# Optimization experiments

Hardware: AMD Instinct MI355X
Metric: run time of the kernel (lower is better)

## Reference

```python
import jax, jax.numpy as jnp
import numpy as np

NUM_HEADS = 16


def setup_inputs() -> dict:
    key = jax.random.key(0)
    k1, k2, k3, k4 = jax.random.split(key, 4)
    B, S, D = 2, 2048, 1024
    x = jax.random.normal(k1, (B, S, D), dtype=jnp.float32)
    W_qkv = jax.random.normal(k2, (D, 3 * D), dtype=jnp.float32) * (1.0 / np.sqrt(D))
    b_qkv = jax.random.normal(k3, (3 * D,), dtype=jnp.float32) * 0.02
    W_out = jax.random.normal(k4, (D, D), dtype=jnp.float32) * (1.0 / np.sqrt(D))
    return {"x": x, "W_qkv": W_qkv, "b_qkv": b_qkv, "W_out": W_out}


def reference(x, W_qkv, b_qkv, W_out):
    B, S, D = x.shape
    H = NUM_HEADS
    Hd = D // H
    scale = 1.0 / np.sqrt(Hd)

    qkv = x @ W_qkv + b_qkv                      # [B, S, 3D]
    q, k, v = jnp.split(qkv, 3, axis=-1)
    # [B, H, S, Hd]
    q = q.reshape(B, S, H, Hd).transpose(0, 2, 1, 3)
    k = k.reshape(B, S, H, Hd).transpose(0, 2, 1, 3)
    v = v.reshape(B, S, H, Hd).transpose(0, 2, 1, 3)

    scores = jnp.einsum('bhqd,bhkd->bhqk', q, k) * scale  # [B, H, S, S]
    causal = jnp.triu(jnp.full((S, S), -jnp.inf, dtype=scores.dtype), k=1)
    scores = scores + causal
    attn = jax.nn.softmax(scores.astype(jnp.float32), axis=-1).astype(q.dtype)

    ctx = jnp.einsum('bhqk,bhkd->bhqd', attn, v)           # [B, H, S, Hd]
    ctx = ctx.transpose(0, 2, 1, 3).reshape(B, S, D)
    return ctx @ W_out
```

## Files before the change

kernel.cpp:

```cpp
#include <hip/hip_runtime.h>
#include <hip/hip_bf16.h>

typedef __bf16 bf16x8 __attribute__((ext_vector_type(8)));
typedef float f32x4 __attribute__((ext_vector_type(4)));

typedef __attribute__((address_space(1))) void gv_t;
typedef __attribute__((address_space(3))) void lv_t;

__device__ __forceinline__ unsigned short f2bf(float f) {
    unsigned int u = __float_as_uint(f);
    unsigned int r = (u + 0x7fffu + ((u >> 16) & 1u)) >> 16;
    return (unsigned short)r;
}

__device__ __forceinline__ unsigned int cvt_pk_bf16(float a, float b) {
    unsigned int r;
    asm("v_cvt_pk_bf16_f32 %0, %1, %2" : "=v"(r) : "v"(a), "v"(b));
    return r;
}

__global__ void convert_f32_bf16(const float* __restrict__ in,
                                 unsigned short* __restrict__ out, int n4) {
    int i = blockIdx.x * blockDim.x + threadIdx.x;
    if (i >= n4) return;
    float4 v = reinterpret_cast<const float4*>(in)[i];
    ushort4 o;
    o.x = f2bf(v.x); o.y = f2bf(v.y); o.z = f2bf(v.z); o.w = f2bf(v.w);
    reinterpret_cast<ushort4*>(out)[i] = o;
}

__global__ void transpose_convert(const float* __restrict__ in,
                                  unsigned short* __restrict__ out,
                                  int K, int N) {
    __shared__ float t[32][33];
    int n0 = blockIdx.x * 32, k0 = blockIdx.y * 32;
    t[threadIdx.y][threadIdx.x] = in[(size_t)(k0 + threadIdx.y) * N + (n0 + threadIdx.x)];
    __syncthreads();
    out[(size_t)(n0 + threadIdx.y) * K + (k0 + threadIdx.x)] = f2bf(t[threadIdx.x][threadIdx.y]);
}

template <bool BIAS, bool OUT_BF16, bool QSCALE>
__global__ __launch_bounds__(256) void gemm_bt(const unsigned short* __restrict__ A,
                                               const unsigned short* __restrict__ Bt,
                                               const float* __restrict__ bias,
                                               void* __restrict__ Cv,
                                               int M, int N, int K) {
    __shared__ alignas(16) unsigned short As[128 * 32];
    __shared__ alignas(16) unsigned short Bs[128 * 32];

    const int t = threadIdx.x;
    const int lane = t & 63;
    const int wid = t >> 6;
    const int wr = wid >> 1, wc = wid & 1;
    const int m0 = blockIdx.y * 128, n0 = blockIdx.x * 128;

    f32x4 acc[4][4] = {};

    for (int k0 = 0; k0 < K; k0 += 32) {
#pragma unroll
        for (int i = 0; i < 2; ++i) {
            int c = i * 256 + t;
            int row = c >> 2;
            int col = (c & 3) * 8;
            const unsigned short* ga = A + (size_t)(m0 + row) * K + k0 + col;
            const unsigned short* gb = Bt + (size_t)(n0 + row) * K + k0 + col;
            __builtin_amdgcn_global_load_lds((gv_t*)ga, (lv_t*)(As + c * 8), 16, 0, 0);
            __builtin_amdgcn_global_load_lds((gv_t*)gb, (lv_t*)(Bs + c * 8), 16, 0, 0);
        }
        __syncthreads();

        bf16x8 af[4], bfr[4];
#pragma unroll
        for (int i = 0; i < 4; ++i)
            af[i] = *reinterpret_cast<const bf16x8*>(As + (wr * 64 + i * 16 + (lane & 15)) * 32 + (lane >> 4) * 8);
#pragma unroll
        for (int j = 0; j < 4; ++j)
            bfr[j] = *reinterpret_cast<const bf16x8*>(Bs + (wc * 64 + j * 16 + (lane & 15)) * 32 + (lane >> 4) * 8);
#pragma unroll
        for (int i = 0; i < 4; ++i)
#pragma unroll
            for (int j = 0; j < 4; ++j)
                acc[i][j] = __builtin_amdgcn_mfma_f32_16x16x32_bf16(af[i], bfr[j], acc[i][j], 0, 0, 0);
        __syncthreads();
    }

#pragma unroll
    for (int i = 0; i < 4; ++i) {
        int row = m0 + wr * 64 + i * 16 + (lane >> 4) * 4;
#pragma unroll
        for (int j = 0; j < 4; ++j) {
            int col = n0 + wc * 64 + j * 16 + (lane & 15);
            float bv = 0.0f;
            if (BIAS) bv = bias[col];
#pragma unroll
            for (int r = 0; r < 4; ++r) {
                float v = acc[i][j][r] + bv;
                if constexpr (QSCALE) { if (col < 1024) v *= 0.125f; }
                if constexpr (OUT_BF16)
                    ((unsigned short*)Cv)[(size_t)(row + r) * N + col] = f2bf(v);
                else
                    ((float*)Cv)[(size_t)(row + r) * N + col] = v;
            }
        }
    }
}

__global__ __launch_bounds__(512) void attn_fwd(const unsigned short* __restrict__ qkv,
                                                unsigned short* __restrict__ ctx,
                                                int S) {
    const int TD = 3072, D = 1024;
    __shared__ alignas(16) unsigned short Ks[2][64 * 64];
    __shared__ alignas(16) unsigned short Vt[2][64 * 64];
    __shared__ alignas(16) unsigned short Ps[8][16 * 64];

    const int t = threadIdx.x, lane = t & 63;
    const int w_all = t >> 6;
    const int w_loc = w_all & 3;
    const bool is_hi = (w_all < 4);
    const int l15 = lane & 15, l4 = lane >> 4;
    const int lin = blockIdx.y * 16 + blockIdx.x;
    const int swz = (lin & 7) * 64 + (lin >> 3);
    const int pid = swz & 15;
    const int bh = swz >> 4;
    const int b = bh >> 4, h = bh & 15;
    const int QT_lo = pid, QT_hi = 31 - pid;
    const int QT = is_hi ? QT_hi : QT_lo;

    const size_t base = ((size_t)b * S) * TD + (size_t)h * 64;
    const unsigned short* qp = qkv + base;
    const unsigned short* kp = qkv + base + D;
    const unsigned short* vp = qkv + base + 2 * D;

    bf16x8 aq[2];
    {
        const unsigned short* g = qp + (size_t)(QT * 64 + w_loc * 16 + l15) * TD + l4 * 8;
        aq[0] = *reinterpret_cast<const bf16x8*>(g);
        aq[1] = *reinterpret_cast<const bf16x8*>(g + 32);
    }

    f32x4 oc[4] = {};
    float lR = 0.f;
    const float L2E = 1.44269504f;
    const float MFIX = 12.0f * L2E;

    auto stageK = [&](int j0, int buf) {
        int c = t;
        int row = c >> 3, hh = c & 7;
        const unsigned short* src = kp + (size_t)(j0 * 64 + row) * TD + ((hh ^ (row & 7)) * 8);
        __builtin_amdgcn_global_load_lds((gv_t*)src, (lv_t*)(Ks[buf] + c * 8), 16, 0, 0);
    };
    const int v_hd = (t & 31) * 2, v_kvb = (t >> 5) * 4;
    unsigned int vv[4];
    auto loadV = [&](int j0) {
        const unsigned short* vsrc = vp + (size_t)(j0 * 64 + v_kvb) * TD + v_hd;
#pragma unroll
        for (int e = 0; e < 4; ++e)
            vv[e] = *reinterpret_cast<const unsigned int*>(vsrc + (size_t)e * TD);
    };
    auto writeV = [&](int buf) {
        unsigned int r0a = __builtin_amdgcn_perm(vv[1], vv[0], 0x05040100u);
        unsigned int r0b = __builtin_amdgcn_perm(vv[3], vv[2], 0x05040100u);
        unsigned int r1a = __builtin_amdgcn_perm(vv[1], vv[0], 0x07060302u);
        unsigned int r1b = __builtin_amdgcn_perm(vv[3], vv[2], 0x07060302u);
        int g0 = (v_kvb >> 3) ^ (v_hd & 7);
        int g1 = (v_kvb >> 3) ^ ((v_hd + 1) & 7);
        int sub = v_kvb & 7;
        *reinterpret_cast<uint2*>(Vt[buf] + v_hd * 64 + g0 * 8 + sub) = make_uint2(r0a, r0b);
        *reinterpret_cast<uint2*>(Vt[buf] + (v_hd + 1) * 64 + g1 * 8 + sub) = make_uint2(r1a, r1b);
    };

    auto compute = [&](bool diag, int buf) {
        f32x4 sc[4];
        __builtin_amdgcn_s_setprio(1);
#pragma unroll
        for (int jn = 0; jn < 4; ++jn) {
            f32x4 s = {};
#pragma unroll
            for (int kk = 0; kk < 2; ++kk) {
                int row = jn * 16 + l15;
                int g = (kk * 4 + l4) ^ (l15 & 7);
                bf16x8 ak = *reinterpret_cast<const bf16x8*>(Ks[buf] + row * 64 + g * 8);
                s = __builtin_amdgcn_mfma_f32_16x16x32_bf16(ak, aq[kk], s, 0, 0, 0);
            }
            sc[jn] = s;
        }
        __builtin_amdgcn_s_setprio(0);
        if (diag) {
            int ql = w_loc * 16 + l15;
#pragma unroll
            for (int jn = 0; jn < 4; ++jn)
#pragma unroll
                for (int r = 0; r < 4; ++r)
                    if (jn * 16 + l4 * 4 + r > ql) sc[jn][r] = -1e30f;
        }
        float ps = 0.f;
#pragma unroll
        for (int jn = 0; jn < 4; ++jn) {
            float p0 = exp2f(sc[jn][0] * L2E - MFIX);
            float p1 = exp2f(sc[jn][1] * L2E - MFIX);
            float p2 = exp2f(sc[jn][2] * L2E - MFIX);
            float p3 = exp2f(sc[jn][3] * L2E - MFIX);
            sc[jn][0] = p0; sc[jn][1] = p1; sc[jn][2] = p2; sc[jn][3] = p3;
            ps += (p0 + p1) + (p2 + p3);
        }
        lR += ps;
        const int q = l15;
#pragma unroll
        for (int jn = 0; jn < 4; ++jn) {
            unsigned int lo = cvt_pk_bf16(sc[jn][0], sc[jn][1]);
            unsigned int hi = cvt_pk_bf16(sc[jn][2], sc[jn][3]);
            int kv0 = jn * 16 + l4 * 4;
            int g = (kv0 >> 3) ^ (q & 7);
            *reinterpret_cast<uint2*>(Ps[w_all] + q * 64 + g * 8 + (kv0 & 7)) = make_uint2(lo, hi);
        }
        __builtin_amdgcn_s_setprio(1);
#pragma unroll
        for (int kk = 0; kk < 2; ++kk) {
            int gq = (kk * 4 + l4) ^ (q & 7);
            bf16x8 bp = *reinterpret_cast<const bf16x8*>(Ps[w_all] + q * 64 + gq * 8);
#pragma unroll
            for (int jc = 0; jc < 4; ++jc) {
                int hdrow = jc * 16 + l15;
                int gv = (kk * 4 + l4) ^ (l15 & 7);
                bf16x8 av = *reinterpret_cast<const bf16x8*>(Vt[buf] + hdrow * 64 + gv * 8);
                oc[jc] = __builtin_amdgcn_mfma_f32_16x16x32_bf16(av, bp, oc[jc], 0, 0, 0);
            }
        }
        __builtin_amdgcn_s_setprio(0);
    };

    stageK(0, 0);
    loadV(0);
    writeV(0);
    __syncthreads();

    for (int j0 = 0; j0 <= QT_hi; ++j0) {
        const int cur = j0 & 1, nxt = cur ^ 1;
        const bool have_next = (j0 < QT_hi);
        if (have_next) {
            stageK(j0 + 1, nxt);
            loadV(j0 + 1);
        }
        if (j0 <= QT) compute(j0 == QT, cur);
        if (have_next) writeV(nxt);
        __syncthreads();
    }

    {
        lR += __shfl_xor(lR, 16);
        lR += __shfl_xor(lR, 32);
        float inv = 1.0f / lR;
        size_t qg = (size_t)QT * 64 + w_loc * 16 + l15;
        unsigned short* crow = ctx + ((size_t)b * S + qg) * D + h * 64;
#pragma unroll
        for (int jc = 0; jc < 4; ++jc) {
            unsigned int pk0 = cvt_pk_bf16(oc[jc][0] * inv, oc[jc][1] * inv);
            unsigned int pk1 = cvt_pk_bf16(oc[jc][2] * inv, oc[jc][3] * inv);
            *reinterpret_cast<uint2*>(crow + jc * 16 + l4 * 4) = make_uint2(pk0, pk1);
        }
    }
}

extern "C" void kernel_launch(void* const* d_in, const int* in_sizes, int n_in,
                              void* d_out, int out_size, void* d_ws, size_t ws_size,
                              hipStream_t stream) {
    const float* x = (const float*)d_in[0];
    const float* Wqkv = (const float*)d_in[1];
    const float* bqkv = (const float*)d_in[2];
    const float* Wout = (const float*)d_in[3];
    float* out = (float*)d_out;

    const int B = 2, S = 2048, D = 1024, TD = 3072;
    const int M = B * S;

    char* ws = (char*)d_ws;
    unsigned short* x_bf  = (unsigned short*)(ws);
    unsigned short* wqkvT = (unsigned short*)(ws + 8388608);
    unsigned short* woutT = (unsigned short*)(ws + 14680064);
    unsigned short* qkv   = (unsigned short*)(ws + 16777216);
    unsigned short* ctx   = (unsigned short*)(ws + 41943040);

    convert_f32_bf16<<<dim3((M * D / 4 + 255) / 256), dim3(256), 0, stream>>>(x, x_bf, M * D / 4);
    transpose_convert<<<dim3(TD / 32, D / 32), dim3(32, 32), 0, stream>>>(Wqkv, wqkvT, D, TD);
    transpose_convert<<<dim3(D / 32, D / 32), dim3(32, 32), 0, stream>>>(Wout, woutT, D, D);

    gemm_bt<true, true, true><<<dim3(TD / 128, M / 128), dim3(256), 0, stream>>>(
        x_bf, wqkvT, bqkv, (void*)qkv, M, TD, D);

    attn_fwd<<<dim3(16, 32), dim3(512), 0, stream>>>(qkv, ctx, S);

    gemm_bt<false, false, false><<<dim3(D / 128, M / 128), dim3(256), 0, stream>>>(
        ctx, woutT, nullptr, (void*)out, M, D, D);
}
```

Baseline: 128.6 us.

## Process two KV tiles per pipeline stage in attention kernel

Doubles the K/V shared-memory stage to 128 rows, so each loop iteration stages two 64-row KV tiles and runs two compute passes between barriers. This halves the number of __syncthreads and loop iterations and gives each global load more compute to hide behind. V loads become 8 rows per thread with 16-byte LDS writes. In exchange, LDS use doubles, which may lower occupancy, and per-thread register pressure rises from the larger V staging buffer.

Measured after the change: 126.2 us. No clear change (-1.9%).

```diff
diff --git a/kernel.cpp b/kernel.cpp
--- a/kernel.cpp
+++ b/kernel.cpp
@@ -109,8 +109,8 @@
                                                 unsigned short* __restrict__ ctx,
                                                 int S) {
     const int TD = 3072, D = 1024;
-    __shared__ alignas(16) unsigned short Ks[2][64 * 64];
-    __shared__ alignas(16) unsigned short Vt[2][64 * 64];
+    __shared__ alignas(16) unsigned short Ks[2][128 * 64];
+    __shared__ alignas(16) unsigned short Vt[2][128 * 64];
     __shared__ alignas(16) unsigned short Ps[8][16 * 64];
 
     const int t = threadIdx.x, lane = t & 63;
@@ -143,33 +143,46 @@
     const float L2E = 1.44269504f;
     const float MFIX = 12.0f * L2E;
 
-    auto stageK = [&](int j0, int buf) {
-        int c = t;
-        int row = c >> 3, hh = c & 7;
-        const unsigned short* src = kp + (size_t)(j0 * 64 + row) * TD + ((hh ^ (row & 7)) * 8);
-        __builtin_amdgcn_global_load_lds((gv_t*)src, (lv_t*)(Ks[buf] + c * 8), 16, 0, 0);
+    auto stageK2 = [&](int j0, int buf) {
+        int j1 = min(j0 + 1, QT_hi);
+#pragma unroll
+        for (int rnd = 0; rnd < 2; ++rnd) {
+            int c = rnd * 512 + t;
+            int row = c >> 3, hh = c & 7;
+            int gkv = (row < 64) ? (j0 * 64 + row) : (j1 * 64 + (row & 63));
+            const unsigned short* src = kp + (size_t)gkv * TD + ((hh ^ (row & 7)) * 8);
+            __builtin_amdgcn_global_load_lds((gv_t*)src, (lv_t*)(Ks[buf] + c * 8), 16, 0, 0);
+        }
     };
-    const int v_hd = (t & 31) * 2, v_kvb = (t >> 5) * 4;
-    unsigned int vv[4];
-    auto loadV = [&](int j0) {
-        const unsigned short* vsrc = vp + (size_t)(j0 * 64 + v_kvb) * TD + v_hd;
-#pragma unroll
-        for (int e = 0; e < 4; ++e)
+    const int v_hd = (t & 31) * 2, v_kvb = (t >> 5) * 8;
+    unsigned int vv[8];
+    auto loadV2 = [&](int j0) {
+        int j1 = min(j0 + 1, QT_hi);
+        int gkv = (v_kvb < 64) ? (j0 * 64 + v_kvb) : (j1 * 64 + (v_kvb & 63));
+        const unsigned short* vsrc = vp + (size_t)gkv * TD + v_hd;
+#pragma unroll
+        for (int e = 0; e < 8; ++e)
             vv[e] = *reinterpret_cast<const unsigned int*>(vsrc + (size_t)e * TD);
     };
-    auto writeV = [&](int buf) {
-        unsigned int r0a = __builtin_amdgcn_perm(vv[1], vv[0], 0x05040100u);
-        unsigned int r0b = __builtin_amdgcn_perm(vv[3], vv[2], 0x05040100u);
-        unsigned int r1a = __builtin_amdgcn_perm(vv[1], vv[0], 0x07060302u);
-        unsigned int r1b = __builtin_amdgcn_perm(vv[3], vv[2], 0x07060302u);
-        int g0 = (v_kvb >> 3) ^ (v_hd & 7);
-        int g1 = (v_kvb >> 3) ^ ((v_hd + 1) & 7);
-        int sub = v_kvb & 7;
-        *reinterpret_cast<uint2*>(Vt[buf] + v_hd * 64 + g0 * 8 + sub) = make_uint2(r0a, r0b);
-        *reinterpret_cast<uint2*>(Vt[buf] + (v_hd + 1) * 64 + g1 * 8 + sub) = make_uint2(r1a, r1b);
+    auto writeV2 = [&](int buf) {
+        unsigned int r0[4], r1[4];
+#pragma unroll
+        for (int i = 0; i < 4; ++i) {
+            r0[i] = __builtin_amdgcn_perm(vv[2 * i + 1], vv[2 * i], 0x05040100u);
+            r1[i] = __builtin_amdgcn_perm(vv[2 * i + 1], vv[2 * i], 0x07060302u);
+        }
+        int half = v_kvb >> 6;
+        int kv0 = v_kvb & 63;
+        int g0 = (kv0 >> 3) ^ (v_hd & 7);
+        int g1 = (kv0 >> 3) ^ ((v_hd + 1) & 7);
+        unsigned short* vb = Vt[buf] + half * 4096;
+        *reinterpret_cast<uint4*>(vb + v_hd * 64 + g0 * 8) = make_uint4(r0[0], r0[1], r0[2], r0[3]);
+        *reinterpret_cast<uint4*>(vb + (v_hd + 1) * 64 + g1 * 8) = make_uint4(r1[0], r1[1], r1[2], r1[3]);
     };
 
-    auto compute = [&](bool diag, int buf) {
+    auto compute = [&](bool diag, int buf, int half) {
+        const unsigned short* Kb = Ks[buf] + half * 4096;
+        const unsigned short* Vb = Vt[buf] + half * 4096;
         f32x4 sc[4];
         __builtin_amdgcn_s_setprio(1);
 #pragma unroll
@@ -179,7 +192,7 @@
             for (int kk = 0; kk < 2; ++kk) {
                 int row = jn * 16 + l15;
                 int g = (kk * 4 + l4) ^ (l15 & 7);
-                bf16x8 ak = *reinterpret_cast<const bf16x8*>(Ks[buf] + row * 64 + g * 8);
+                bf16x8 ak = *reinterpret_cast<const bf16x8*>(Kb + row * 64 + g * 8);
                 s = __builtin_amdgcn_mfma_f32_16x16x32_bf16(ak, aq[kk], s, 0, 0, 0);
             }
             sc[jn] = s;
@@ -222,27 +235,28 @@
             for (int jc = 0; jc < 4; ++jc) {
                 int hdrow = jc * 16 + l15;
                 int gv = (kk * 4 + l4) ^ (l15 & 7);
-                bf16x8 av = *reinterpret_cast<const bf16x8*>(Vt[buf] + hdrow * 64 + gv * 8);
+                bf16x8 av = *reinterpret_cast<const bf16x8*>(Vb + hdrow * 64 + gv * 8);
                 oc[jc] = __builtin_amdgcn_mfma_f32_16x16x32_bf16(av, bp, oc[jc], 0, 0, 0);
             }
         }
         __builtin_amdgcn_s_setprio(0);
     };
 
-    stageK(0, 0);
-    loadV(0);
-    writeV(0);
+    stageK2(0, 0);
+    loadV2(0);
+    writeV2(0);
     __syncthreads();
 
-    for (int j0 = 0; j0 <= QT_hi; ++j0) {
-        const int cur = j0 & 1, nxt = cur ^ 1;
-        const bool have_next = (j0 < QT_hi);
+    for (int jj = 0; jj <= QT_hi; jj += 2) {
+        const int cur = (jj >> 1) & 1, nxt = cur ^ 1;
+        const bool have_next = (jj + 2 <= QT_hi);
         if (have_next) {
-            stageK(j0 + 1, nxt);
-            loadV(j0 + 1);
-        }
-        if (j0 <= QT) compute(j0 == QT, cur);
-        if (have_next) writeV(nxt);
+            stageK2(jj + 2, nxt);
+            loadV2(jj + 2);
+        }
+        if (jj <= QT) compute(jj == QT, cur, 0);
+        if (jj + 1 <= QT) compute(jj + 1 == QT, cur, 1);
+        if (have_next) writeV2(nxt);
         __syncthreads();
     }
 
```
